# Kernel tuning notes

Measured on AMD Instinct MI355X. Metric: run time of the kernel, lower is better.

Reference implementation:

```python
import jax, jax.numpy as jnp
import numpy as np

N_SRC = 100000
N_DST = 100000
E = 1600000
D_IN = 64
D_OUT = 64
LN_EPS = 1e-5


def setup_inputs() -> dict:
    key = jax.random.key(0)
    k1, k2, k3, k4, k5 = jax.random.split(key, 5)
    feat = jax.random.normal(k1, (N_SRC, D_IN), dtype=jnp.float32)
    edge_src = jax.random.randint(k2, (E,), 0, N_SRC, dtype=jnp.int32)
    edge_dst = jax.random.randint(k3, (E,), 0, N_DST, dtype=jnp.int32)
    W_w = jax.random.normal(k4, (D_IN, D_OUT), dtype=jnp.float32) * (1.0 / np.sqrt(D_IN))
    film_w = jax.random.normal(k5, (D_IN, 2 * D_OUT), dtype=jnp.float32) * (1.0 / np.sqrt(D_IN))
    ln_scale = jnp.ones((D_OUT,), dtype=jnp.float32)
    ln_bias = jnp.zeros((D_OUT,), dtype=jnp.float32)
    return {"feat": feat, "edge_src": edge_src, "edge_dst": edge_dst,
            "W_w": W_w, "film_w": film_w, "ln_scale": ln_scale, "ln_bias": ln_bias}


def reference(feat, edge_src, edge_dst, W_w, film_w, ln_scale, ln_bias):
    # messages = relu(gamma * (feat @ W) + beta), gamma/beta from film linear
    msg = feat @ W_w                                  # [N_src, D_OUT]
    film = feat @ film_w                              # [N_src, 2*D_OUT]
    gamma, beta = film[:, :D_OUT], film[:, D_OUT:]
    msg = jax.nn.relu(gamma * msg + beta)             # [N_src, D_OUT]
    # copy_u + sum: scatter-sum messages from source nodes to destinations
    h = jax.ops.segment_sum(msg[edge_src], edge_dst, num_segments=N_DST)  # [N_dst, D_OUT]
    # LayerNorm over feature dim (dropout is identity in eval)
    mu = jnp.mean(h, axis=-1, keepdims=True)
    var = jnp.var(h, axis=-1, keepdims=True)
    out = (h - mu) * jax.lax.rsqrt(var + LN_EPS) * ln_scale + ln_bias
    return out
```

## Files before the change

kernel.cpp:

```cpp
#include <hip/hip_runtime.h>

constexpr int N_SRC = 100000;
constexpr int N_DST = 100000;
constexpr int E     = 1600000;
constexpr int D     = 64;
constexpr float LN_EPS = 1e-5f;

constexpr int NCHUNK = 512;
constexpr int CHUNK  = E / NCHUNK;
constexpr int BROWS  = 128;
constexpr int NBK    = (N_DST + BROWS - 1) / BROWS;
constexpr int MAXB   = 4096;
constexpr int FB     = 72;

typedef __attribute__((ext_vector_type(8))) short bf16x8;
typedef __attribute__((ext_vector_type(4))) float f32x4;

__device__ inline unsigned short bfh(float x) {
    union { float f; unsigned u; } c; c.f = x; return (unsigned short)(c.u >> 16);
}
__device__ inline float bff(unsigned short b) {
    union { unsigned u; float f; } c; c.u = (unsigned)b << 16; return c.f;
}
__device__ inline float asf(unsigned u) {
    union { unsigned u; float f; } c; c.u = u; return c.f;
}
__device__ inline unsigned short bfrne(float x) {
    union { float f; unsigned u; } c; c.f = x;
    unsigned u = c.u + (0x7FFFu + ((c.u >> 16) & 1u));
    return (unsigned short)(u >> 16);
}

__global__ __launch_bounds__(256) void k_film(const float* __restrict__ feat,
                                              const float* __restrict__ Ww,
                                              const float* __restrict__ Fw,
                                              unsigned short* __restrict__ msgb) {
    __shared__ unsigned short wl[6 * 64 * FB];

    const int tid  = threadIdx.x;
    const int lane = tid & 63;
    const int wid  = tid >> 6;
    const int m    = lane & 15;
    const int kg   = lane >> 4;
    const int mrow0 = (blockIdx.x * 4 + wid) * 32;

    bf16x8 ahi[2][2], alo[2][2];
#pragma unroll
    for (int mt = 0; mt < 2; ++mt) {
        const int rbase = mrow0 + mt * 16 + m;
        const int r = (rbase < N_SRC) ? rbase : 0;
#pragma unroll
        for (int ks = 0; ks < 2; ++ks) {
            const float* p = feat + (size_t)r * 64 + ks * 32 + kg * 8;
            const float4 x0 = *reinterpret_cast<const float4*>(p);
            const float4 x1 = *reinterpret_cast<const float4*>(p + 4);
            const float a[8] = {x0.x, x0.y, x0.z, x0.w, x1.x, x1.y, x1.z, x1.w};
            bf16x8 h, l;
#pragma unroll
            for (int j = 0; j < 8; ++j) {
                const unsigned short hb = bfh(a[j]);
                h[j] = (short)hb;
                l[j] = (short)bfh(a[j] - bff(hb));
            }
            ahi[mt][ks] = h; alo[mt][ks] = l;
        }
    }

    for (int task = tid; task < 1536; task += 256) {
        const int g  = task & 7;
        const int n  = (task >> 3) & 63;
        const int mu = task >> 9;
        const float* src;
        int stride;
        if (mu == 0)      { src = Ww + n;       stride = 64;  }
        else if (mu == 1) { src = Fw + n;       stride = 128; }
        else              { src = Fw + 64 + n;  stride = 128; }
        bf16x8 h, l;
#pragma unroll
        for (int j = 0; j < 8; ++j) {
            const float v = src[(size_t)(8 * g + j) * stride];
            const unsigned short hb = bfh(v);
            h[j] = (short)hb;
            l[j] = (short)bfh(v - bff(hb));
        }
        *reinterpret_cast<bf16x8*>(&wl[(2 * mu + 0) * 64 * FB + n * FB + g * 8]) = h;
        *reinterpret_cast<bf16x8*>(&wl[(2 * mu + 1) * 64 * FB + n * FB + g * 8]) = l;
    }
    __syncthreads();

    const f32x4 zero = {0.f, 0.f, 0.f, 0.f};

#pragma unroll
    for (int t = 0; t < 4; ++t) {
        f32x4 am[2], ag[2], ab[2];
#pragma unroll
        for (int i = 0; i < 2; ++i) { am[i] = zero; ag[i] = zero; ab[i] = zero; }

#pragma unroll
        for (int ks = 0; ks < 2; ++ks) {
            const int n = t * 16 + m;
            const int koff = ks * 32 + kg * 8;
            const int base = n * FB + koff;
            const bf16x8 wmh = *reinterpret_cast<const bf16x8*>(&wl[0 * 64 * FB + base]);
            const bf16x8 wml = *reinterpret_cast<const bf16x8*>(&wl[1 * 64 * FB + base]);
            const bf16x8 wgh = *reinterpret_cast<const bf16x8*>(&wl[2 * 64 * FB + base]);
            const bf16x8 wgl = *reinterpret_cast<const bf16x8*>(&wl[3 * 64 * FB + base]);
            const bf16x8 wbh = *reinterpret_cast<const bf16x8*>(&wl[4 * 64 * FB + base]);
            const bf16x8 wbl = *reinterpret_cast<const bf16x8*>(&wl[5 * 64 * FB + base]);
#pragma unroll
            for (int mt = 0; mt < 2; ++mt) {
                am[mt] = __builtin_amdgcn_mfma_f32_16x16x32_bf16(ahi[mt][ks], wmh, am[mt], 0, 0, 0);
                am[mt] = __builtin_amdgcn_mfma_f32_16x16x32_bf16(ahi[mt][ks], wml, am[mt], 0, 0, 0);
                am[mt] = __builtin_amdgcn_mfma_f32_16x16x32_bf16(alo[mt][ks], wmh, am[mt], 0, 0, 0);
                ag[mt] = __builtin_amdgcn_mfma_f32_16x16x32_bf16(ahi[mt][ks], wgh, ag[mt], 0, 0, 0);
                ag[mt] = __builtin_amdgcn_mfma_f32_16x16x32_bf16(ahi[mt][ks], wgl, ag[mt], 0, 0, 0);
                ag[mt] = __builtin_amdgcn_mfma_f32_16x16x32_bf16(alo[mt][ks], wgh, ag[mt], 0, 0, 0);
                ab[mt] = __builtin_amdgcn_mfma_f32_16x16x32_bf16(ahi[mt][ks], wbh, ab[mt], 0, 0, 0);
                ab[mt] = __builtin_amdgcn_mfma_f32_16x16x32_bf16(ahi[mt][ks], wbl, ab[mt], 0, 0, 0);
                ab[mt] = __builtin_amdgcn_mfma_f32_16x16x32_bf16(alo[mt][ks], wbh, ab[mt], 0, 0, 0);
            }
        }

#pragma unroll
        for (int mt = 0; mt < 2; ++mt) {
            const int rb = mrow0 + mt * 16;
            if (rb < N_SRC) {
#pragma unroll
                for (int r4 = 0; r4 < 4; ++r4) {
                    const int row = rb + kg * 4 + r4;
                    const float o = fmaxf(ag[mt][r4] * am[mt][r4] + ab[mt][r4], 0.f);
                    msgb[(size_t)row * 64 + t * 16 + m] = bfrne(o);
                }
            }
        }
    }
}

__global__ __launch_bounds__(256) void k_hist1(const int* __restrict__ edst,
                                               int* __restrict__ H) {
    __shared__ int hl[NBK];
    for (int i = threadIdx.x; i < NBK; i += 256) hl[i] = 0;
    __syncthreads();
    const int c = blockIdx.x;
    const int e0 = c * CHUNK;
    for (int e = e0 + threadIdx.x; e < e0 + CHUNK; e += 256)
        atomicAdd(&hl[edst[e] >> 7], 1);
    __syncthreads();
    for (int i = threadIdx.x; i < NBK; i += 256) H[i * NCHUNK + c] = hl[i];
}

__global__ __launch_bounds__(512) void k_scanH(int* __restrict__ H,
                                               int* __restrict__ bstart) {
    const int k = blockIdx.x;
    const int c = threadIdx.x;
    const int lane = c & 63;
    const int wid = c >> 6;
    const int v = H[k * NCHUNK + c];
    int x = v;
#pragma unroll
    for (int o = 1; o < 64; o <<= 1) { int y = __shfl_up(x, o); if (lane >= o) x += y; }
    __shared__ int wsum[8];
    if (lane == 63) wsum[wid] = x;
    __syncthreads();
    int add = 0;
    for (int w = 0; w < wid; ++w) add += wsum[w];
    const int incl = x + add;
    H[k * NCHUNK + c] = incl - v;
    if (c == NCHUNK - 1) bstart[k] = incl;
}

__global__ __launch_bounds__(64) void k_h3(int* __restrict__ bstart) {
    const int lane = threadIdx.x;
    int running = 0;
    for (int b = 0; b < NBK; b += 64) {
        const int idx = b + lane;
        const int v = (idx < NBK) ? bstart[idx] : 0;
        int x = v;
#pragma unroll
        for (int o = 1; o < 64; o <<= 1) { int y = __shfl_up(x, o); if (lane >= o) x += y; }
        if (idx < NBK) bstart[idx] = running + x - v;
        running += __shfl(x, 63);
    }
    if (lane == 0) bstart[NBK] = E;
}

__global__ __launch_bounds__(256) void k_pairs(const int* __restrict__ esrc,
                                               const int* __restrict__ edst,
                                               const int* __restrict__ H,
                                               const int* __restrict__ bstart,
                                               unsigned* __restrict__ pairs) {
    __shared__ int curs[NBK];
    const int c = blockIdx.x;
    for (int i = threadIdx.x; i < NBK; i += 256) curs[i] = bstart[i] + H[i * NCHUNK + c];
    __syncthreads();
    const int e0 = c * CHUNK;
    for (int e = e0 + threadIdx.x; e < e0 + CHUNK; e += 256) {
        const int d = edst[e];
        const int s = esrc[e];
        const int k = d >> 7;
        const int pos = atomicAdd(&curs[k], 1);
        pairs[pos] = ((unsigned)(d & 127) << 24) | (unsigned)s;
    }
}

__global__ __launch_bounds__(512) void k_reduce2(const unsigned short* __restrict__ msgb,
                                                 const unsigned* __restrict__ pairs,
                                                 const int* __restrict__ bstart,
                                                 const float* __restrict__ sc,
                                                 const float* __restrict__ bi,
                                                 float* __restrict__ out) {
    __shared__ int srcs[MAXB];
    __shared__ int cnt[BROWS];
    __shared__ int off[BROWS];
    __shared__ int cur[BROWS];

    const int k = blockIdx.x;
    const int tid = threadIdx.x;
    const int lane = tid & 63;
    const int wid = tid >> 6;
    const int s0 = bstart[k];
    const int s1 = bstart[k + 1];

    for (int i = tid; i < BROWS; i += 512) cnt[i] = 0;
    __syncthreads();

    for (int i = s0 + tid; i < s1; i += 512) atomicAdd(&cnt[pairs[i] >> 24], 1);
    __syncthreads();

    if (tid < 64) {
        const int a = cnt[lane];
        const int b = cnt[64 + lane];
        int xa = a, xb = b;
#pragma unroll
        for (int o = 1; o < 64; o <<= 1) {
            int ya = __shfl_up(xa, o); if (lane >= o) xa += ya;
            int yb = __shfl_up(xb, o); if (lane >= o) xb += yb;
        }
        const int tot_a = __shfl(xa, 63);
        off[lane]      = xa - a;
        off[64 + lane] = tot_a + xb - b;
        cur[lane]      = off[lane];
        cur[64 + lane] = off[64 + lane];
    }
    __syncthreads();

    for (int i = s0 + tid; i < s1; i += 512) {
        const unsigned p = pairs[i];
        const int pos = atomicAdd(&cur[p >> 24], 1);
        if (pos < MAXB) srcs[pos] = (int)(p & 0x1FFFFu);
    }
    __syncthreads();

    const int q = lane >> 4;
    const int c = lane & 15;

    for (int r = wid; r < BROWS; r += 8) {
        const int dst = k * BROWS + r;
        if (dst >= N_DST) break;
        const int rn = cnt[r];
        const int ro = off[r];

        float ax = 0.f, ay = 0.f, az = 0.f, aw = 0.f;
        for (int b0 = 0; b0 < rn; b0 += 32) {
            int sj[8]; bool okv[8];
#pragma unroll
            for (int j = 0; j < 8; ++j) {
                const int ei = b0 + 4 * j + q;
                okv[j] = ei < rn;
                sj[j] = srcs[ro + min(ei, rn - 1)];
            }
#pragma unroll
            for (int j = 0; j < 8; ++j) {
                if (b0 + 4 * j >= rn) break;
                const uint2 v = *reinterpret_cast<const uint2*>(
                    msgb + (size_t)sj[j] * D + c * 4);
                const unsigned msk = okv[j] ? 0xFFFFFFFFu : 0u;
                const unsigned vx = v.x & msk, vy = v.y & msk;
                ax += asf(vx << 16);
                ay += asf(vx & 0xFFFF0000u);
                az += asf(vy << 16);
                aw += asf(vy & 0xFFFF0000u);
            }
        }

        ax += __shfl_xor(ax, 32); ay += __shfl_xor(ay, 32);
        az += __shfl_xor(az, 32); aw += __shfl_xor(aw, 32);
        ax += __shfl_xor(ax, 16); ay += __shfl_xor(ay, 16);
        az += __shfl_xor(az, 16); aw += __shfl_xor(aw, 16);

        float s = (ax + ay) + (az + aw);
#pragma unroll
        for (int o = 8; o > 0; o >>= 1) s += __shfl_xor(s, o);
        const float mu = s * (1.0f / D);
        const float dx = ax - mu, dy = ay - mu, dz = az - mu, dw = aw - mu;
        float s2 = (dx * dx + dy * dy) + (dz * dz + dw * dw);
#pragma unroll
        for (int o = 8; o > 0; o >>= 1) s2 += __shfl_xor(s2, o);
        const float rs = rsqrtf(s2 * (1.0f / D) + LN_EPS);

        if (lane < 16) {
            const float4 scv = *reinterpret_cast<const float4*>(sc + c * 4);
            const float4 biv = *reinterpret_cast<const float4*>(bi + c * 4);
            float4 o4;
            o4.x = dx * rs * scv.x + biv.x;
            o4.y = dy * rs * scv.y + biv.y;
            o4.z = dz * rs * scv.z + biv.z;
            o4.w = dw * rs * scv.w + biv.w;
            *reinterpret_cast<float4*>(out + (size_t)dst * D + c * 4) = o4;
        }
    }
}

extern "C" void kernel_launch(void* const* d_in, const int* in_sizes, int n_in,
                              void* d_out, int out_size, void* d_ws, size_t ws_size,
                              hipStream_t stream) {
    const float* feat = (const float*)d_in[0];
    const int*   esrc = (const int*)d_in[1];
    const int*   edst = (const int*)d_in[2];
    const float* Ww   = (const float*)d_in[3];
    const float* Fw   = (const float*)d_in[4];
    const float* sc   = (const float*)d_in[5];
    const float* bi   = (const float*)d_in[6];
    float* out = (float*)d_out;

    char* ws = (char*)d_ws;
    unsigned short* msgb = (unsigned short*)(ws);
    unsigned* pairs  = (unsigned*)(ws + 26u * 1024 * 1024);
    int*      H      = (int*)(ws + 33u * 1024 * 1024);
    int*      bstart = (int*)(ws + 35u * 1024 * 1024);

    k_film  <<<782, 256, 0, stream>>>(feat, Ww, Fw, msgb);
    k_hist1 <<<NCHUNK, 256, 0, stream>>>(edst, H);
    k_scanH <<<NBK, 512, 0, stream>>>(H, bstart);
    k_h3    <<<1, 64, 0, stream>>>(bstart);
    k_pairs <<<NCHUNK, 256, 0, stream>>>(esrc, edst, H, bstart, pairs);
    k_reduce2<<<NBK, 512, 0, stream>>>(msgb, pairs, bstart, sc, bi, out);
}
```

Before: 205.6 us.

## Fuse histogram, scans and pair scatter into one kernel with grid barriers

Merges the four sorting kernels (histogram, per-bucket scan, bucket-start scan, pair scatter) into a single persistent kernel of NBK blocks synchronised by atomic-counter grid barriers. The chunk count now equals the bucket count (782), so the scan runs four elements per thread. The goal is to cut kernel launch gaps and intermediate dispatches. It relies on all 782 blocks being co-resident for the spin barriers, which risks deadlock if they are not. The reduce loop also drops the masked prefetch in favour of a zeroed padding row in msgb, and the weight-load task order in k_film changes.

```diff
diff --git a/kernel.cpp b/kernel.cpp
--- a/kernel.cpp
+++ b/kernel.cpp
@@ -6,12 +6,13 @@
 constexpr int D     = 64;
 constexpr float LN_EPS = 1e-5f;
 
-constexpr int NCHUNK = 512;
-constexpr int CHUNK  = E / NCHUNK;
 constexpr int BROWS  = 128;
 constexpr int NBK    = (N_DST + BROWS - 1) / BROWS;
+constexpr int NCHUNK = NBK;
+constexpr int CHUNKB = E / NCHUNK;
 constexpr int MAXB   = 4096;
 constexpr int FB     = 72;
+constexpr int ZROW   = N_SRC;
 
 typedef __attribute__((ext_vector_type(8))) short bf16x8;
 typedef __attribute__((ext_vector_type(4))) float f32x4;
@@ -34,7 +35,8 @@
 __global__ __launch_bounds__(256) void k_film(const float* __restrict__ feat,
                                               const float* __restrict__ Ww,
                                               const float* __restrict__ Fw,
-                                              unsigned short* __restrict__ msgb) {
+                                              unsigned short* __restrict__ msgb,
+                                              int* __restrict__ ctr) {
     __shared__ unsigned short wl[6 * 64 * FB];
 
     const int tid  = threadIdx.x;
@@ -44,6 +46,13 @@
     const int kg   = lane >> 4;
     const int mrow0 = (blockIdx.x * 4 + wid) * 32;
 
+    if (blockIdx.x == 0) {
+        if (tid < 64) msgb[(size_t)ZROW * 64 + tid] = 0;
+        if (tid >= 64 && tid < 67)
+            __hip_atomic_store(&ctr[tid - 64], 0, __ATOMIC_RELAXED,
+                               __HIP_MEMORY_SCOPE_AGENT);
+    }
+
     bf16x8 ahi[2][2], alo[2][2];
 #pragma unroll
     for (int mt = 0; mt < 2; ++mt) {
@@ -67,8 +76,8 @@
     }
 
     for (int task = tid; task < 1536; task += 256) {
-        const int g  = task & 7;
-        const int n  = (task >> 3) & 63;
+        const int n  = task & 63;
+        const int g  = (task >> 6) & 7;
         const int mu = task >> 9;
         const float* src;
         int stride;
@@ -99,8 +108,7 @@
 #pragma unroll
         for (int ks = 0; ks < 2; ++ks) {
             const int n = t * 16 + m;
-            const int koff = ks * 32 + kg * 8;
-            const int base = n * FB + koff;
+            const int base = n * FB + ks * 32 + kg * 8;
             const bf16x8 wmh = *reinterpret_cast<const bf16x8*>(&wl[0 * 64 * FB + base]);
             const bf16x8 wml = *reinterpret_cast<const bf16x8*>(&wl[1 * 64 * FB + base]);
             const bf16x8 wgh = *reinterpret_cast<const bf16x8*>(&wl[2 * 64 * FB + base]);
@@ -136,69 +144,87 @@
     }
 }
 
-__global__ __launch_bounds__(256) void k_hist1(const int* __restrict__ edst,
-                                               int* __restrict__ H) {
-    __shared__ int hl[NBK];
-    for (int i = threadIdx.x; i < NBK; i += 256) hl[i] = 0;
-    __syncthreads();
-    const int c = blockIdx.x;
-    const int e0 = c * CHUNK;
-    for (int e = e0 + threadIdx.x; e < e0 + CHUNK; e += 256)
-        atomicAdd(&hl[edst[e] >> 7], 1);
-    __syncthreads();
-    for (int i = threadIdx.x; i < NBK; i += 256) H[i * NCHUNK + c] = hl[i];
-}
-
-__global__ __launch_bounds__(512) void k_scanH(int* __restrict__ H,
-                                               int* __restrict__ bstart) {
-    const int k = blockIdx.x;
-    const int c = threadIdx.x;
-    const int lane = c & 63;
-    const int wid = c >> 6;
-    const int v = H[k * NCHUNK + c];
-    int x = v;
-#pragma unroll
-    for (int o = 1; o < 64; o <<= 1) { int y = __shfl_up(x, o); if (lane >= o) x += y; }
-    __shared__ int wsum[8];
-    if (lane == 63) wsum[wid] = x;
-    __syncthreads();
-    int add = 0;
-    for (int w = 0; w < wid; ++w) add += wsum[w];
-    const int incl = x + add;
-    H[k * NCHUNK + c] = incl - v;
-    if (c == NCHUNK - 1) bstart[k] = incl;
-}
-
-__global__ __launch_bounds__(64) void k_h3(int* __restrict__ bstart) {
-    const int lane = threadIdx.x;
-    int running = 0;
-    for (int b = 0; b < NBK; b += 64) {
-        const int idx = b + lane;
-        const int v = (idx < NBK) ? bstart[idx] : 0;
-        int x = v;
+__device__ inline void gbar(int* ctr, int nblk) {
+    __syncthreads();
+    if (threadIdx.x == 0) {
+        __threadfence();
+        atomicAdd(ctr, 1);
+        while (atomicAdd(ctr, 0) < nblk) { __builtin_amdgcn_s_sleep(4); }
+        __threadfence();
+    }
+    __syncthreads();
+}
+
+__global__ __launch_bounds__(256) void k_sort(const int* __restrict__ esrc,
+                                              const int* __restrict__ edst,
+                                              int* __restrict__ H,
+                                              int* __restrict__ bstart,
+                                              unsigned* __restrict__ pairs,
+                                              int* __restrict__ ctr) {
+    __shared__ int sh[NBK];
+    const int tid  = threadIdx.x;
+    const int lane = tid & 63;
+    const int wid  = tid >> 6;
+    const int c    = blockIdx.x;
+    const int e0   = c * CHUNKB;
+    const int e1   = (c == NCHUNK - 1) ? E : e0 + CHUNKB;
+
+    for (int k = tid; k < NBK; k += 256) sh[k] = 0;
+    __syncthreads();
+    for (int e = e0 + tid; e < e1; e += 256) atomicAdd(&sh[edst[e] >> 7], 1);
+    __syncthreads();
+    for (int k = tid; k < NBK; k += 256) H[k * NCHUNK + c] = sh[k];
+
+    gbar(ctr + 0, NCHUNK);
+
+    {
+        const int b = blockIdx.x;
+        const int base = 4 * tid;
+        int v0 = (base + 0 < NCHUNK) ? H[b * NCHUNK + base + 0] : 0;
+        int v1 = (base + 1 < NCHUNK) ? H[b * NCHUNK + base + 1] : 0;
+        int v2 = (base + 2 < NCHUNK) ? H[b * NCHUNK + base + 2] : 0;
+        int v3 = (base + 3 < NCHUNK) ? H[b * NCHUNK + base + 3] : 0;
+        const int p1 = v0 + v1, p2 = p1 + v2, tt = p2 + v3;
+        int x = tt;
 #pragma unroll
         for (int o = 1; o < 64; o <<= 1) { int y = __shfl_up(x, o); if (lane >= o) x += y; }
-        if (idx < NBK) bstart[idx] = running + x - v;
-        running += __shfl(x, 63);
-    }
-    if (lane == 0) bstart[NBK] = E;
-}
-
-__global__ __launch_bounds__(256) void k_pairs(const int* __restrict__ esrc,
-                                               const int* __restrict__ edst,
-                                               const int* __restrict__ H,
-                                               const int* __restrict__ bstart,
-                                               unsigned* __restrict__ pairs) {
-    __shared__ int curs[NBK];
-    const int c = blockIdx.x;
-    for (int i = threadIdx.x; i < NBK; i += 256) curs[i] = bstart[i] + H[i * NCHUNK + c];
-    __syncthreads();
-    const int e0 = c * CHUNK;
-    for (int e = e0 + threadIdx.x; e < e0 + CHUNK; e += 256) {
+        __syncthreads();
+        if (lane == 63) sh[wid] = x;
+        __syncthreads();
+        int add = 0;
+        for (int w = 0; w < wid; ++w) add += sh[w];
+        const int excl = add + x - tt;
+        if (base + 0 < NCHUNK) H[b * NCHUNK + base + 0] = excl;
+        if (base + 1 < NCHUNK) H[b * NCHUNK + base + 1] = excl + v0;
+        if (base + 2 < NCHUNK) H[b * NCHUNK + base + 2] = excl + p1;
+        if (base + 3 < NCHUNK) H[b * NCHUNK + base + 3] = excl + p2;
+        if (tid == 255) bstart[b] = excl + tt;
+    }
+
+    gbar(ctr + 1, NCHUNK);
+
+    if (blockIdx.x == 0 && tid < 64) {
+        int running = 0;
+        for (int b = 0; b < NBK; b += 64) {
+            const int idx = b + lane;
+            const int v = (idx < NBK) ? bstart[idx] : 0;
+            int x = v;
+#pragma unroll
+            for (int o = 1; o < 64; o <<= 1) { int y = __shfl_up(x, o); if (lane >= o) x += y; }
+            if (idx < NBK) bstart[idx] = running + x - v;
+            running += __shfl(x, 63);
+        }
+        if (lane == 0) bstart[NBK] = E;
+    }
+
+    gbar(ctr + 2, NCHUNK);
+
+    for (int k = tid; k < NBK; k += 256) sh[k] = bstart[k] + H[k * NCHUNK + c];
+    __syncthreads();
+    for (int e = e0 + tid; e < e1; e += 256) {
         const int d = edst[e];
         const int s = esrc[e];
-        const int k = d >> 7;
-        const int pos = atomicAdd(&curs[k], 1);
+        const int pos = atomicAdd(&sh[d >> 7], 1);
         pairs[pos] = ((unsigned)(d & 127) << 24) | (unsigned)s;
     }
 }
@@ -262,24 +288,17 @@
 
         float ax = 0.f, ay = 0.f, az = 0.f, aw = 0.f;
         for (int b0 = 0; b0 < rn; b0 += 32) {
-            int sj[8]; bool okv[8];
-#pragma unroll
-            for (int j = 0; j < 8; ++j) {
-                const int ei = b0 + 4 * j + q;
-                okv[j] = ei < rn;
-                sj[j] = srcs[ro + min(ei, rn - 1)];
-            }
 #pragma unroll
             for (int j = 0; j < 8; ++j) {
                 if (b0 + 4 * j >= rn) break;
+                const int ei = b0 + 4 * j + q;
+                const int sj = (ei < rn) ? srcs[ro + ei] : ZROW;
                 const uint2 v = *reinterpret_cast<const uint2*>(
-                    msgb + (size_t)sj[j] * D + c * 4);
-                const unsigned msk = okv[j] ? 0xFFFFFFFFu : 0u;
-                const unsigned vx = v.x & msk, vy = v.y & msk;
-                ax += asf(vx << 16);
-                ay += asf(vx & 0xFFFF0000u);
-                az += asf(vy << 16);
-                aw += asf(vy & 0xFFFF0000u);
+                    msgb + (size_t)sj * D + c * 4);
+                ax += asf(v.x << 16);
+                ay += asf(v.x & 0xFFFF0000u);
+                az += asf(v.y << 16);
+                aw += asf(v.y & 0xFFFF0000u);
             }
         }
 
@@ -327,12 +346,10 @@
     unsigned short* msgb = (unsigned short*)(ws);
     unsigned* pairs  = (unsigned*)(ws + 26u * 1024 * 1024);
     int*      H      = (int*)(ws + 33u * 1024 * 1024);
-    int*      bstart = (int*)(ws + 35u * 1024 * 1024);
-
-    k_film  <<<782, 256, 0, stream>>>(feat, Ww, Fw, msgb);
-    k_hist1 <<<NCHUNK, 256, 0, stream>>>(edst, H);
-    k_scanH <<<NBK, 512, 0, stream>>>(H, bstart);
-    k_h3    <<<1, 64, 0, stream>>>(bstart);
-    k_pairs <<<NCHUNK, 256, 0, stream>>>(esrc, edst, H, bstart, pairs);
+    int*      bstart = (int*)(ws + 36u * 1024 * 1024);
+    int*      ctr    = (int*)(ws + 36u * 1024 * 1024 + 4096);
+
+    k_film   <<<782, 256, 0, stream>>>(feat, Ww, Fw, msgb, ctr);
+    k_sort   <<<NCHUNK, 256, 0, stream>>>(esrc, edst, H, bstart, pairs, ctr);
     k_reduce2<<<NBK, 512, 0, stream>>>(msgb, pairs, bstart, sc, bi, out);
 }
```

New measurement: 421.3 us. +104.9%, slower.
